# Performance work log

Measured on AMD Instinct MI355X. Metric: run time of the kernel, lower is better.

The kernel has to match this reference:

```python
import jax, jax.numpy as jnp
import numpy as np

N, E, D, H, C = 50000, 600000, 128, 8, 16
NEG_SLOPE = 0.2


def setup_inputs() -> dict:
    key = jax.random.key(0)
    k = jax.random.split(key, 6)
    x = jax.random.normal(k[0], (N, D), dtype=jnp.float32)
    edge_index = jax.random.randint(k[1], (2, E), 0, N, dtype=jnp.int64)
    # GATConv params (glorot-style scale)
    W = jax.random.normal(k[2], (D, H * C), dtype=jnp.float32) * (1.0 / np.sqrt(D))
    a_src = jax.random.normal(k[3], (H, C), dtype=jnp.float32) * (1.0 / np.sqrt(C))
    a_dst = jax.random.normal(k[4], (H, C), dtype=jnp.float32) * (1.0 / np.sqrt(C))
    bias = jnp.zeros((H * C,), dtype=jnp.float32)
    return {"x": x, "edge_index": edge_index, "W": W, "a_src": a_src, "a_dst": a_dst, "bias": bias}


def reference(x, edge_index, W, a_src, a_dst, bias):
    # Eval-mode GATConv: dropout disabled. add_self_loops=True (PyG default).
    n = x.shape[0]
    loops = jnp.arange(n, dtype=edge_index.dtype)
    src = jnp.concatenate([edge_index[0], loops])  # [E+N]
    dst = jnp.concatenate([edge_index[1], loops])

    h = (x @ W).reshape(n, H, C)                       # [N,H,C]
    alpha_s = jnp.einsum('nhc,hc->nh', h, a_src)       # [N,H]
    alpha_d = jnp.einsum('nhc,hc->nh', h, a_dst)

    e = alpha_s[src] + alpha_d[dst]                    # [E+N,H]
    e = jnp.where(e > 0, e, NEG_SLOPE * e)             # LeakyReLU

    # segment softmax over incoming edges of each destination node
    e_max = jax.ops.segment_max(e, dst, num_segments=n)   # [N,H]
    e_exp = jnp.exp(e - e_max[dst])
    e_sum = jax.ops.segment_sum(e_exp, dst, num_segments=n)
    alpha = e_exp / (e_sum[dst] + 1e-16)               # [E+N,H]

    msg = alpha[:, :, None] * h[src]                   # [E+N,H,C]
    out = jax.ops.segment_sum(msg, dst, num_segments=n)  # [N,H,C]
    return out.reshape(n, H * C) + bias
```

## Files before the change

### kernel.cpp

```cpp
#include <hip/hip_runtime.h>
#include <hip/hip_fp16.h>

#define HD 8
#define CD 16
#define DIM 128
#define NEG_SLOPE 0.2f
#define RSHIFT 13
#define RSIZE (1<<RSHIFT)
#define SEG 32
#define SCAT_SHIFT 12

typedef __attribute__((ext_vector_type(8))) _Float16 f16x8;
typedef __attribute__((ext_vector_type(4))) float    f32x4;

static __device__ __forceinline__ float lrelu(float v){ return v > 0.f ? v : NEG_SLOPE*v; }

__global__ __launch_bounds__(256) void k_wprep(const float* __restrict__ W, __half* __restrict__ Wt){
  int idx = blockIdx.x*256 + threadIdx.x;
  if (idx < DIM*DIM){
    int k = idx >> 7, c = idx & 127;
    Wt[(size_t)c*DIM + k] = __float2half(W[idx]);
  }
}

__global__ __launch_bounds__(256, 3) void k_gemm(const float* __restrict__ x,
    const __half* __restrict__ Wt, const float* __restrict__ a_src_g, const float* __restrict__ a_dst_g,
    __half* __restrict__ hout, float* __restrict__ as_o, float* __restrict__ ad_o, int N)
{
  __shared__ __half xs[64*136];
  const int tid  = threadIdx.x;
  const int lane = tid & 63;
  const int wv   = tid >> 6;
  const long nbase = (long)blockIdx.x * 64;

  #pragma unroll
  for (int it = 0; it < 8; ++it){
    int lin = it*1024 + tid*4;
    int row = lin >> 7, col = lin & 127;
    long node = nbase + row;
    float4 v = make_float4(0.f,0.f,0.f,0.f);
    if (node < N) v = *(const float4*)(x + node*DIM + col);
    __half2* dstp = (__half2*)(xs + row*136 + col);
    dstp[0] = __floats2half2_rn(v.x, v.y);
    dstp[1] = __floats2half2_rn(v.z, v.w);
  }
  __syncthreads();

  const int lrow = lane & 15;
  const int g    = lane >> 4;

  f16x8 af[4];
  #pragma unroll
  for (int ks = 0; ks < 4; ++ks)
    af[ks] = *(const f16x8*)(xs + (wv*16 + lrow)*136 + ks*32 + g*8);

  f32x4 accs[8];
  #pragma unroll
  for (int t = 0; t < 8; ++t){
    f32x4 acc = {0.f,0.f,0.f,0.f};
    #pragma unroll
    for (int ks = 0; ks < 4; ++ks){
      f16x8 bf = *(const f16x8*)(Wt + (size_t)(t*16 + lrow)*DIM + ks*32 + g*8);
      acc = __builtin_amdgcn_mfma_f32_16x16x32_f16(af[ks], bf, acc, 0, 0, 0);
    }
    accs[t] = acc;
  }

  #pragma unroll
  for (int t = 0; t < 8; ++t)
    #pragma unroll
    for (int i = 0; i < 4; ++i)
      xs[(wv*16 + g*4 + i)*136 + t*16 + lrow] = __float2half(accs[t][i]);
  __syncthreads();

  #pragma unroll
  for (int j = 0; j < 4; ++j){
    int idx = j*256 + tid;
    int row = idx >> 4, seg = idx & 15;
    long node = nbase + row;
    if (node < N){
      uint4 v = *(const uint4*)((const char*)xs + row*272 + seg*16);
      *(uint4*)(hout + node*DIM + seg*8) = v;
    }
  }
  #pragma unroll
  for (int j = 0; j < 2; ++j){
    int idx = j*256 + tid;
    int row = idx >> 3, hd = idx & 7;
    long node = nbase + row;
    if (node < N){
      const __half* hp = xs + row*136 + hd*16;
      float ps = 0.f, pd = 0.f;
      #pragma unroll
      for (int cc = 0; cc < 16; ++cc){
        float hv = __half2float(hp[cc]);
        ps += hv * a_src_g[hd*16 + cc];
        pd += hv * a_dst_g[hd*16 + cc];
      }
      as_o[node*HD + hd] = ps;
      ad_o[node*HD + hd] = pd;
    }
  }
}

__global__ __launch_bounds__(256) void k_count(const int* __restrict__ dst,
                                               int* __restrict__ cnt_seg, int* __restrict__ slot,
                                               int E, int N, int Eseg){
  __shared__ int hist[RSIZE];
  const int p = blockIdx.x / SEG;
  const int s = blockIdx.x % SEG;
  for (int i = threadIdx.x; i < RSIZE; i += 256) hist[i] = 0;
  __syncthreads();
  const int lo = p << RSHIFT;
  const int end = min((s+1)*Eseg, E);
  for (int e = s*Eseg + threadIdx.x; e < end; e += 256){
    unsigned r = (unsigned)(dst[e] - lo);
    if (r < RSIZE)
      slot[e] = atomicAdd(&hist[r], 1);
  }
  __syncthreads();
  for (int i = threadIdx.x; i < RSIZE; i += 256){
    int node = lo + i;
    if (node < N) cnt_seg[(size_t)s*N + node] = hist[i];
  }
}

__global__ __launch_bounds__(256) void k_scan1(const int* __restrict__ cnt_seg, int* __restrict__ bsum,
                                               int chunk, int N){
  __shared__ int tmp[256];
  int t = threadIdx.x;
  int i = blockIdx.x*chunk + t;
  int v = 0;
  if (t < chunk && i < N){
    #pragma unroll
    for (int s = 0; s < SEG; ++s) v += cnt_seg[(size_t)s*N + i];
  }
  tmp[t] = v; __syncthreads();
  for (int off = 128; off > 0; off >>= 1){
    if (t < off) tmp[t] += tmp[t+off];
    __syncthreads();
  }
  if (t == 0) bsum[blockIdx.x] = tmp[0];
}

__global__ __launch_bounds__(256) void k_scan2(int* __restrict__ bsum, int* __restrict__ row_ofs, int N){
  __shared__ int tmp[256];
  int t = threadIdx.x;
  int v = bsum[t];
  tmp[t] = v; __syncthreads();
  for (int off = 1; off < 256; off <<= 1){
    int u = (t >= off) ? tmp[t-off] : 0;
    __syncthreads();
    tmp[t] += u;
    __syncthreads();
  }
  bsum[t] = tmp[t] - v;
  if (t == 255) row_ofs[N] = tmp[255];
}

__global__ __launch_bounds__(256) void k_scan3(const int* __restrict__ cnt_seg, const int* __restrict__ bsum,
                                               int* __restrict__ row_ofs, int* __restrict__ cofs,
                                               int chunk, int N){
  __shared__ int tmp[256];
  int t = threadIdx.x;
  int i = blockIdx.x*chunk + t;
  int v[SEG]; int tot = 0;
  if (t < chunk && i < N){
    #pragma unroll
    for (int s = 0; s < SEG; ++s){ v[s] = cnt_seg[(size_t)s*N + i]; tot += v[s]; }
  }
  tmp[t] = tot; __syncthreads();
  for (int off = 1; off < 256; off <<= 1){
    int u = (t >= off) ? tmp[t-off] : 0;
    __syncthreads();
    tmp[t] += u;
    __syncthreads();
  }
  int excl = tmp[t] - tot;
  int bbase = bsum[blockIdx.x];
  if (t < chunk && i < N){
    int run = bbase + excl;
    row_ofs[i] = run;
    #pragma unroll
    for (int s = 0; s < SEG; ++s){ cofs[(size_t)s*N + i] = run; run += v[s]; }
  }
}

__global__ void k_scatter(const int* __restrict__ src, const int* __restrict__ dst,
                          const int* __restrict__ slot, const int* __restrict__ cofs,
                          int* __restrict__ csr_src, int E, int N, int Eseg, int npass){
  int e = blockIdx.x*256 + threadIdx.x;
  if (e >= E) return;
  int d = dst[e];
  int s = src[e];
  int seg = e / Eseg;
  int pos = cofs[(size_t)seg*N + d] + slot[e];
  int myp = d >> SCAT_SHIFT;
  for (int p = 0; p < npass; ++p){
    if (myp == p)
      csr_src[pos] = s;
    asm volatile("" ::: "memory");
  }
}

__global__ __launch_bounds__(256) void k_aggr(const __half* __restrict__ h,
    const float* __restrict__ as_, const float* __restrict__ ad_,
    const int* __restrict__ row_ofs, const int* __restrict__ csr_src,
    const float* __restrict__ bias, float* __restrict__ out, int N)
{
  const int n = blockIdx.x*4 + (threadIdx.x >> 6);
  if (n >= N) return;
  const int t  = threadIdx.x & 63;
  const int hb = t >> 3;
  const int sl = t & 7;
  const int off = t*2;

  const float ad_n = ad_[(size_t)n*HD + hb];
  const float w_self = __expf(lrelu(as_[(size_t)n*HD + hb] + ad_n));

  float sum = w_self;
  float2 hv = __half22float2(*(const __half2*)(h + (size_t)n*DIM + off));
  float2 acc; acc.x = w_self*hv.x; acc.y = w_self*hv.y;

  const int ofs = row_ofs[n];
  const int deg = row_ofs[n+1] - ofs;

  for (int jb = 0; jb < deg; jb += 16){
    const int c = deg - jb;
    int s[16];
    #pragma unroll
    for (int q = 0; q < 16; ++q){
      int sq = csr_src[ofs + jb + q];
      s[q] = (q < c) ? sq : n;
    }

    __half2 hq[16];
    #pragma unroll
    for (int q = 0; q < 16; ++q)
      hq[q] = *(const __half2*)(h + (size_t)s[q]*DIM + off);

    float v0 = __expf(lrelu(as_[(size_t)s[sl]*HD + hb] + ad_n));
    float v1 = __expf(lrelu(as_[(size_t)s[sl+8]*HD + hb] + ad_n));
    const float wv0 = (sl     < c) ? v0 : 0.f;
    const float wv1 = (sl + 8 < c) ? v1 : 0.f;

    #pragma unroll
    for (int q = 0; q < 8; ++q){
      float w0 = __shfl(wv0, hb*8 + q);
      float2 hf = __half22float2(hq[q]);
      sum += w0; acc.x += w0*hf.x; acc.y += w0*hf.y;
    }
    #pragma unroll
    for (int q = 0; q < 8; ++q){
      float w1 = __shfl(wv1, hb*8 + q);
      float2 hf = __half22float2(hq[8+q]);
      sum += w1; acc.x += w1*hf.x; acc.y += w1*hf.y;
    }
  }

  const float2 bv = *(const float2*)(bias + off);
  const float inv = 1.0f / (sum + 1e-16f);
  float2 o;
  o.x = acc.x*inv + bv.x;
  o.y = acc.y*inv + bv.y;
  *(float2*)(out + (size_t)n*DIM + off) = o;
}

extern "C" void kernel_launch(void* const* d_in, const int* in_sizes, int n_in,
                              void* d_out, int out_size, void* d_ws, size_t ws_size,
                              hipStream_t stream)
{
  const float* x     = (const float*)d_in[0];
  const int*   ei    = (const int*)  d_in[1];
  const float* W     = (const float*)d_in[2];
  const float* a_src = (const float*)d_in[3];
  const float* a_dst = (const float*)d_in[4];
  const float* bias  = (const float*)d_in[5];
  float* out = (float*)d_out;

  const int N = in_sizes[0] / DIM;
  const int E = in_sizes[1] / 2;
  const int* src = ei;
  const int* dst = ei + E;

  char* w = (char*)d_ws;
  __half* h    = (__half*)w; w += (size_t)N*DIM*2;
  __half* Wt   = (__half*)w; w += (size_t)DIM*DIM*2;
  float* as_   = (float*)w; w += (size_t)N*HD*4;
  float* ad_   = (float*)w; w += (size_t)N*HD*4;
  int* csr_src = (int*)w;   w += (size_t)(E+16)*4;
  int* slot    = (int*)w;   w += (size_t)E*4;
  int* cnt_seg = (int*)w;   w += (size_t)SEG*N*4;
  int* cofs    = (int*)w;   w += (size_t)SEG*N*4;
  int* bsum    = (int*)w;   w += 256*4;
  int* row_ofs = (int*)w;   w += (size_t)(N+1)*4;

  const int chunk = (N + 255) / 256;
  const int RB    = (N + RSIZE-1) >> RSHIFT;
  const int Eseg  = (E + SEG-1) / SEG;
  const int gb    = (N + 63) / 64;
  const int npass = (N >> SCAT_SHIFT) + 1;

  hipLaunchKernelGGL(k_wprep,   dim3(64),          dim3(256), 0, stream, W, Wt);
  hipLaunchKernelGGL(k_gemm,    dim3(gb),          dim3(256), 0, stream, x, Wt, a_src, a_dst, h, as_, ad_, N);
  hipLaunchKernelGGL(k_count,   dim3(RB*SEG),      dim3(256), 0, stream, dst, cnt_seg, slot, E, N, Eseg);
  hipLaunchKernelGGL(k_scan1,   dim3(256),         dim3(256), 0, stream, cnt_seg, bsum, chunk, N);
  hipLaunchKernelGGL(k_scan2,   dim3(1),           dim3(256), 0, stream, bsum, row_ofs, N);
  hipLaunchKernelGGL(k_scan3,   dim3(256),         dim3(256), 0, stream, cnt_seg, bsum, row_ofs, cofs, chunk, N);
  hipLaunchKernelGGL(k_scatter, dim3((E+255)/256), dim3(256), 0, stream, src, dst, slot, cofs, csr_src, E, N, Eseg, npass);
  hipLaunchKernelGGL(k_aggr,    dim3((N+3)/4),     dim3(256), 0, stream, h, as_, ad_, row_ofs, csr_src, bias, out, N);
}
```

Before: 117.0 us.

## Fuse destination histogram count into GEMM launch with packed 16-bit counters

The degree-count kernel is folded into the GEMM kernel as extra blocks, so the counting work runs concurrently with the projection GEMM instead of after it. The histogram now packs two 16-bit counters per shared-memory word, which doubles the node range per block (RSHIFT 14) within the same shared memory, and segment counts are stored as unsigned shorts to halve that traffic. This saves a launch and a serial dependency, but the union sharing LDS with the GEMM tile may affect occupancy. Counts per segment are limited to 65535.

```diff
diff --git a/kernel.cpp b/kernel.cpp
--- a/kernel.cpp
+++ b/kernel.cpp
@@ -5,7 +5,7 @@
 #define CD 16
 #define DIM 128
 #define NEG_SLOPE 0.2f
-#define RSHIFT 13
+#define RSHIFT 14
 #define RSIZE (1<<RSHIFT)
 #define SEG 32
 #define SCAT_SHIFT 12
@@ -23,15 +23,45 @@
   }
 }
 
-__global__ __launch_bounds__(256, 3) void k_gemm(const float* __restrict__ x,
+__global__ __launch_bounds__(256, 3) void k_gc(const float* __restrict__ x,
     const __half* __restrict__ Wt, const float* __restrict__ a_src_g, const float* __restrict__ a_dst_g,
-    __half* __restrict__ hout, float* __restrict__ as_o, float* __restrict__ ad_o, int N)
+    __half* __restrict__ hout, float* __restrict__ as_o, float* __restrict__ ad_o, int N,
+    const int* __restrict__ dst, unsigned short* __restrict__ cnt_seg, int* __restrict__ slot,
+    int E, int Eseg, int gb)
 {
-  __shared__ __half xs[64*136];
+  __shared__ union { __half xs[64*136]; unsigned int hist[RSIZE/2]; } sm;
+  const int b = blockIdx.x;
+
+  if (b >= gb){
+    const int cb = b - gb;
+    const int p = cb / SEG;
+    const int s = cb % SEG;
+    for (int i = threadIdx.x; i < RSIZE/2; i += 256) sm.hist[i] = 0;
+    __syncthreads();
+    const int lo = p << RSHIFT;
+    const int end = min((s+1)*Eseg, E);
+    for (int e = s*Eseg + threadIdx.x; e < end; e += 256){
+      unsigned r = (unsigned)(dst[e] - lo);
+      if (r < RSIZE){
+        unsigned sh = (r & 1u) << 4;
+        unsigned old = atomicAdd(&sm.hist[r >> 1], 1u << sh);
+        slot[e] = (int)((old >> sh) & 0xffffu);
+      }
+    }
+    __syncthreads();
+    for (int i = threadIdx.x; i < RSIZE; i += 256){
+      int node = lo + i;
+      if (node < N)
+        cnt_seg[(size_t)s*N + node] =
+          (unsigned short)((sm.hist[i >> 1] >> ((i & 1u) << 4)) & 0xffffu);
+    }
+    return;
+  }
+
   const int tid  = threadIdx.x;
   const int lane = tid & 63;
   const int wv   = tid >> 6;
-  const long nbase = (long)blockIdx.x * 64;
+  const long nbase = (long)b * 64;
 
   #pragma unroll
   for (int it = 0; it < 8; ++it){
@@ -40,7 +70,7 @@
     long node = nbase + row;
     float4 v = make_float4(0.f,0.f,0.f,0.f);
     if (node < N) v = *(const float4*)(x + node*DIM + col);
-    __half2* dstp = (__half2*)(xs + row*136 + col);
+    __half2* dstp = (__half2*)(sm.xs + row*136 + col);
     dstp[0] = __floats2half2_rn(v.x, v.y);
     dstp[1] = __floats2half2_rn(v.z, v.w);
   }
@@ -52,7 +82,7 @@
   f16x8 af[4];
   #pragma unroll
   for (int ks = 0; ks < 4; ++ks)
-    af[ks] = *(const f16x8*)(xs + (wv*16 + lrow)*136 + ks*32 + g*8);
+    af[ks] = *(const f16x8*)(sm.xs + (wv*16 + lrow)*136 + ks*32 + g*8);
 
   f32x4 accs[8];
   #pragma unroll
@@ -70,7 +100,7 @@
   for (int t = 0; t < 8; ++t)
     #pragma unroll
     for (int i = 0; i < 4; ++i)
-      xs[(wv*16 + g*4 + i)*136 + t*16 + lrow] = __float2half(accs[t][i]);
+      sm.xs[(wv*16 + g*4 + i)*136 + t*16 + lrow] = __float2half(accs[t][i]);
   __syncthreads();
 
   #pragma unroll
@@ -79,7 +109,7 @@
     int row = idx >> 4, seg = idx & 15;
     long node = nbase + row;
     if (node < N){
-      uint4 v = *(const uint4*)((const char*)xs + row*272 + seg*16);
+      uint4 v = *(const uint4*)((const char*)sm.xs + row*272 + seg*16);
       *(uint4*)(hout + node*DIM + seg*8) = v;
     }
   }
@@ -89,7 +119,7 @@
     int row = idx >> 3, hd = idx & 7;
     long node = nbase + row;
     if (node < N){
-      const __half* hp = xs + row*136 + hd*16;
+      const __half* hp = sm.xs + row*136 + hd*16;
       float ps = 0.f, pd = 0.f;
       #pragma unroll
       for (int cc = 0; cc < 16; ++cc){
@@ -103,30 +133,8 @@
   }
 }
 
-__global__ __launch_bounds__(256) void k_count(const int* __restrict__ dst,
-                                               int* __restrict__ cnt_seg, int* __restrict__ slot,
-                                               int E, int N, int Eseg){
-  __shared__ int hist[RSIZE];
-  const int p = blockIdx.x / SEG;
-  const int s = blockIdx.x % SEG;
-  for (int i = threadIdx.x; i < RSIZE; i += 256) hist[i] = 0;
-  __syncthreads();
-  const int lo = p << RSHIFT;
-  const int end = min((s+1)*Eseg, E);
-  for (int e = s*Eseg + threadIdx.x; e < end; e += 256){
-    unsigned r = (unsigned)(dst[e] - lo);
-    if (r < RSIZE)
-      slot[e] = atomicAdd(&hist[r], 1);
-  }
-  __syncthreads();
-  for (int i = threadIdx.x; i < RSIZE; i += 256){
-    int node = lo + i;
-    if (node < N) cnt_seg[(size_t)s*N + node] = hist[i];
-  }
-}
-
-__global__ __launch_bounds__(256) void k_scan1(const int* __restrict__ cnt_seg, int* __restrict__ bsum,
-                                               int chunk, int N){
+__global__ __launch_bounds__(256) void k_scan1(const unsigned short* __restrict__ cnt_seg,
+                                               int* __restrict__ bsum, int chunk, int N){
   __shared__ int tmp[256];
   int t = threadIdx.x;
   int i = blockIdx.x*chunk + t;
@@ -158,7 +166,8 @@
   if (t == 255) row_ofs[N] = tmp[255];
 }
 
-__global__ __launch_bounds__(256) void k_scan3(const int* __restrict__ cnt_seg, const int* __restrict__ bsum,
+__global__ __launch_bounds__(256) void k_scan3(const unsigned short* __restrict__ cnt_seg,
+                                               const int* __restrict__ bsum,
                                                int* __restrict__ row_ofs, int* __restrict__ cofs,
                                                int chunk, int N){
   __shared__ int tmp[256];
@@ -290,7 +299,7 @@
   float* ad_   = (float*)w; w += (size_t)N*HD*4;
   int* csr_src = (int*)w;   w += (size_t)(E+16)*4;
   int* slot    = (int*)w;   w += (size_t)E*4;
-  int* cnt_seg = (int*)w;   w += (size_t)SEG*N*4;
+  unsigned short* cnt_seg = (unsigned short*)w; w += (size_t)SEG*N*2;
   int* cofs    = (int*)w;   w += (size_t)SEG*N*4;
   int* bsum    = (int*)w;   w += 256*4;
   int* row_ofs = (int*)w;   w += (size_t)(N+1)*4;
@@ -302,8 +311,8 @@
   const int npass = (N >> SCAT_SHIFT) + 1;
 
   hipLaunchKernelGGL(k_wprep,   dim3(64),          dim3(256), 0, stream, W, Wt);
-  hipLaunchKernelGGL(k_gemm,    dim3(gb),          dim3(256), 0, stream, x, Wt, a_src, a_dst, h, as_, ad_, N);
-  hipLaunchKernelGGL(k_count,   dim3(RB*SEG),      dim3(256), 0, stream, dst, cnt_seg, slot, E, N, Eseg);
+  hipLaunchKernelGGL(k_gc,      dim3(gb + RB*SEG), dim3(256), 0, stream,
+                     x, Wt, a_src, a_dst, h, as_, ad_, N, dst, cnt_seg, slot, E, Eseg, gb);
   hipLaunchKernelGGL(k_scan1,   dim3(256),         dim3(256), 0, stream, cnt_seg, bsum, chunk, N);
   hipLaunchKernelGGL(k_scan2,   dim3(1),           dim3(256), 0, stream, bsum, row_ofs, N);
   hipLaunchKernelGGL(k_scan3,   dim3(256),         dim3(256), 0, stream, cnt_seg, bsum, row_ofs, cofs, chunk, N);
```

New measurement: 106.1 us. 9.3% less time.
